# Kernel optimization log

Measured on AMD Instinct MI355X. Metric: run time of the kernel, lower is better.

The kernel has to match this reference:

```python
import jax, jax.numpy as jnp
import numpy as np

B, T, N, NF, H, C, E = 4, 16, 4096, 8, 64, 13, 131072
NUM_HEADS = 4


def setup_inputs() -> dict:
    key = jax.random.key(0)
    ks = jax.random.split(key, 32)
    s = 0.05

    def w(k, shape):
        return (jax.random.normal(k, shape, jnp.float32) * s)

    p = {}
    p["node_features"] = jax.random.normal(ks[0], (B, T, N, NF), jnp.float32)
    p["edge_index_seq"] = jax.random.randint(ks[1], (T, 2, E), 0, N)
    # spatial_conv: Linear(NF,H) -> ReLU -> Linear(H,H)
    p["sc_w1"] = w(ks[2], (H, NF)); p["sc_b1"] = w(ks[3], (H,))
    p["sc_w2"] = w(ks[4], (H, H)); p["sc_b2"] = w(ks[5], (H,))
    # 2-layer LSTM (eval mode, dropout inactive); gate order i,f,g,o
    p["w_ih0"] = w(ks[6], (4 * H, H)); p["w_hh0"] = w(ks[7], (4 * H, H))
    p["b_ih0"] = w(ks[8], (4 * H,)); p["b_hh0"] = w(ks[9], (4 * H,))
    p["w_ih1"] = w(ks[10], (4 * H, H)); p["w_hh1"] = w(ks[11], (4 * H, H))
    p["b_ih1"] = w(ks[12], (4 * H,)); p["b_hh1"] = w(ks[13], (4 * H,))
    # MultiheadAttention (packed in-proj like torch)
    p["attn_in_w"] = w(ks[14], (3 * H, H)); p["attn_in_b"] = w(ks[15], (3 * H,))
    p["attn_out_w"] = w(ks[16], (H, H)); p["attn_out_b"] = w(ks[17], (H,))
    # predictor MLP (dropout inactive in eval)
    p["pw1"] = w(ks[18], (2 * H, H)); p["pb1"] = w(ks[19], (2 * H,))
    p["pw2"] = w(ks[20], (H, 2 * H)); p["pb2"] = w(ks[21], (H,))
    p["pw3"] = w(ks[22], (C, H)); p["pb3"] = w(ks[23], (C,))
    return p


def _message_pass(h_t, edges, n_nodes):
    # h_t: [B, N, H]; edges: [2, E]
    src, dst = edges[0], edges[1]
    msgs = h_t[:, src, :]  # gather pre-update embeddings, [B, E, H]
    sums = jax.vmap(lambda m: jax.ops.segment_sum(m, dst, num_segments=n_nodes))(msgs)
    cnt = jax.ops.segment_sum(jnp.ones(dst.shape, h_t.dtype), dst, num_segments=n_nodes)
    mean = sums / jnp.maximum(cnt, 1.0)[None, :, None]
    has_msg = (cnt > 0)[None, :, None]
    return jnp.where(has_msg, (h_t + mean) * 0.5, h_t)


def _lstm_layer(x, wi, wh, bi, bh):
    # x: [M, T, H] -> [M, T, H]
    M = x.shape[0]
    Hh = wh.shape[1]
    xg = x @ wi.T + bi  # precompute input contribution, [M, T, 4H]
    def step(carry, xg_t):
        hp, cp = carry
        g = xg_t + hp @ wh.T + bh
        i, f, gg, o = jnp.split(g, 4, axis=-1)
        i = jax.nn.sigmoid(i); f = jax.nn.sigmoid(f)
        gg = jnp.tanh(gg); o = jax.nn.sigmoid(o)
        c = f * cp + i * gg
        hn = o * jnp.tanh(c)
        return (hn, c), hn
    init = (jnp.zeros((M, Hh), x.dtype), jnp.zeros((M, Hh), x.dtype))
    _, hs = jax.lax.scan(step, init, xg.transpose(1, 0, 2))
    return hs.transpose(1, 0, 2)


def reference(node_features, edge_index_seq, sc_w1, sc_b1, sc_w2, sc_b2,
              w_ih0, w_hh0, b_ih0, b_hh0, w_ih1, w_hh1, b_ih1, b_hh1,
              attn_in_w, attn_in_b, attn_out_w, attn_out_b,
              pw1, pb1, pw2, pb2, pw3, pb3):
    Bs, Ts, Ns, _ = node_features.shape
    Hh = sc_w1.shape[0]

    # spatial conv over all timesteps at once: [B, T, N, H]
    h = jax.nn.relu(node_features @ sc_w1.T + sc_b1) @ sc_w2.T + sc_b2

    # per-timestep gather + segment-mean message passing (memory-bound core)
    def step(_, inp):
        h_t, e_t = inp
        return None, _message_pass(h_t, e_t, Ns)
    _, h_mp = jax.lax.scan(step, None, (h.transpose(1, 0, 2, 3), edge_index_seq))
    spatial_stack = h_mp.transpose(1, 0, 2, 3)  # [B, T, N, H]

    # LSTM over time per (batch, node)
    x = spatial_stack.transpose(0, 2, 1, 3).reshape(Bs * Ns, Ts, Hh)
    x = _lstm_layer(x, w_ih0, w_hh0, b_ih0, b_hh0)
    x = _lstm_layer(x, w_ih1, w_hh1, b_ih1, b_hh1)

    # self-attention (torch MHA, batch_first)
    qkv = x @ attn_in_w.T + attn_in_b
    q, k, v = jnp.split(qkv, 3, axis=-1)
    hd = Hh // NUM_HEADS
    def heads(z):
        return z.reshape(Bs * Ns, Ts, NUM_HEADS, hd).transpose(0, 2, 1, 3)
    q, k, v = heads(q), heads(k), heads(v)
    scores = jnp.einsum('mhqd,mhkd->mhqk', q, k) / np.float32(np.sqrt(hd))
    attn = jax.nn.softmax(scores, axis=-1)
    o = jnp.einsum('mhqk,mhkd->mhqd', attn, v)
    o = o.transpose(0, 2, 1, 3).reshape(Bs * Ns, Ts, Hh)
    o = o @ attn_out_w.T + attn_out_b

    final_hidden = o[:, -1, :]
    z = jax.nn.relu(final_hidden @ pw1.T + pb1)
    z = jax.nn.relu(z @ pw2.T + pb2)
    logits = z @ pw3.T + pb3
    return logits.reshape(Bs, Ns, -1)
```

## Files before the change

kernel.cpp:

```cpp
#include <hip/hip_runtime.h>

#define Bq 4
#define Tq 16
#define Nq 4096
#define NFq 8
#define Hq 64
#define Eq 131072
#define Cq 13
#define Mq (Bq*Nq)

typedef __attribute__((ext_vector_type(8))) short bf16x8;
typedef __attribute__((ext_vector_type(4))) float f32x4;

__device__ __forceinline__ float bf2f(unsigned short u) {
  return __uint_as_float(((unsigned int)u) << 16);
}
__device__ __forceinline__ unsigned short f2bf(float f) {
  unsigned int x = __float_as_uint(f);
  unsigned int r = x + 0x7fff + ((x >> 16) & 1);
  return (unsigned short)(r >> 16);
}
__device__ __forceinline__ float rcpf(float x) {
  float r;
  asm("v_rcp_f32 %0, %1" : "=v"(r) : "v"(x));
  return r;
}
__device__ __forceinline__ float sigf(float x) {
  return rcpf(1.f + __expf(-x));
}
__device__ __forceinline__ float tanh_c(float x) {
  float e = __expf(-2.f * x);
  return 2.f * rcpf(1.f + e) - 1.f;
}
__device__ __forceinline__ unsigned int pk_bf16(float lo, float hi) {
  unsigned int r;
  asm("v_cvt_pk_bf16_f32 %0, %1, %2" : "=v"(r) : "v"(lo), "v"(hi));
  return r;
}
__device__ __forceinline__ float dot2bf(unsigned int a, unsigned int b, float c) {
  float r;
  asm("v_dot2_f32_bf16 %0, %1, %2, %3" : "=v"(r) : "v"(a), "v"(b), "v"(c));
  return r;
}

#define O_BC0  65536
#define O_BC1  65792
#define O_QB   70144
#define O_VB   74304
#define O_B1P  95872

#define WB_AQT  0
#define WB_AWK  4096
#define WB_WVT  8192
#define WB_P1OW 12288
#define WB_P2T  20480
#define WB_P3T  28672
#define WB_TOT  29696

#define AQT_P   0
#define WVT_P   2048
#define P1OW_P  4096
#define P2T_P   8192
#define WAVE_SCR 3648
#define SMEM_ATTN (49152 + 8 * WAVE_SCR)

__global__ __launch_bounds__(256) void k_prep(
    const float* __restrict__ bih0, const float* __restrict__ bhh0,
    const float* __restrict__ bih1, const float* __restrict__ bhh1,
    float* __restrict__ wT) {
  int i = threadIdx.x;
  wT[O_BC0 + i] = bih0[i] + bhh0[i];
  wT[O_BC1 + i] = bih1[i] + bhh1[i];
}

__global__ __launch_bounds__(256) void k_prep_wa(
    const float* __restrict__ wih0, const float* __restrict__ whh0,
    const float* __restrict__ wih1, const float* __restrict__ whh1,
    unsigned short* __restrict__ WA) {
  int i = blockIdx.x * 256 + threadIdx.x;
  int j = i & 7, lane = (i >> 3) & 63, ks = (i >> 9) & 3;
  int mt = (i >> 11) & 15, L = (i >> 15) & 1;
  int rp = 16 * mt + (lane & 15);
  int orig = (rp & 3) * 64 + (rp >> 2);
  int k = 32 * ks + 8 * (lane >> 4) + j;
  const float* w = L ? (k < 64 ? wih1 : whh1) : (k < 64 ? wih0 : whh0);
  WA[i] = f2bf(w[orig * 64 + (k & 63)]);
}

__global__ __launch_bounds__(256) void k_prep2(
    const float* __restrict__ aw, const float* __restrict__ ab,
    const float* __restrict__ pw2, const float* __restrict__ pw3,
    unsigned short* __restrict__ WBu, float* __restrict__ wT) {
  int i = blockIdx.x * 256 + threadIdx.x;
  if (i < 4096) {
    int k = i >> 6, ch = i & 63;
    int pidx = (k >> 1) * 128 + ch * 2 + (k & 1);
    WBu[WB_AQT + pidx] = f2bf(0.25f * aw[ch * 64 + k]);
    WBu[WB_AWK + i]    = f2bf(aw[(64 + k) * 64 + ch]);
    WBu[WB_WVT + pidx] = f2bf(aw[(128 + ch) * 64 + k]);
  }
  {
    int k = i >> 6, j = i & 63;
    int pidx = (k >> 1) * 128 + j * 2 + (k & 1);
    WBu[WB_P2T + pidx] = f2bf(pw2[j * 128 + k]);
  }
  if (i < 1024) {
    int k = i >> 4, c = i & 15;
    int pidx = (k >> 1) * 32 + c * 2 + (k & 1);
    WBu[WB_P3T + pidx] = (c < 13) ? f2bf(pw3[c * 64 + k]) : (unsigned short)0;
  }
  if (i < 64) {
    wT[O_QB + i] = 0.25f * ab[i];
    wT[O_VB + i] = ab[128 + i];
  }
}

__global__ __launch_bounds__(256) void k_prep3(
    const float* __restrict__ pw1, const float* __restrict__ ow,
    const float* __restrict__ ob, const float* __restrict__ pb1,
    unsigned short* __restrict__ WBu, float* __restrict__ wT) {
  int i = blockIdx.x * 256 + threadIdx.x;
  int j = i >> 6, k = i & 63;
  float s0 = 0.f, s1 = 0.f, s2 = 0.f, s3 = 0.f;
  for (int m2 = 0; m2 < 64; m2 += 4) {
    s0 += pw1[j * 64 + m2]     * ow[m2 * 64 + k];
    s1 += pw1[j * 64 + m2 + 1] * ow[(m2 + 1) * 64 + k];
    s2 += pw1[j * 64 + m2 + 2] * ow[(m2 + 2) * 64 + k];
    s3 += pw1[j * 64 + m2 + 3] * ow[(m2 + 3) * 64 + k];
  }
  WBu[WB_P1OW + (k >> 1) * 256 + j * 2 + (k & 1)] = f2bf((s0 + s1) + (s2 + s3));
  if (k == 0) {
    float b = pb1[j];
    for (int m2 = 0; m2 < 64; ++m2) b += pw1[j * 64 + m2] * ob[m2];
    wT[O_B1P + j] = b;
  }
}

__global__ __launch_bounds__(256) void k_enc(
    const float* __restrict__ nf, const float* __restrict__ w1,
    const float* __restrict__ b1, const float* __restrict__ w2,
    const float* __restrict__ b2, unsigned short* __restrict__ henc) {
  __shared__ float xr[64][9];
  __shared__ float w1l[64][8];
  __shared__ float b1l[64];
  __shared__ float w2l[4096];
  __shared__ float b2l[64];
  __shared__ float h1l[64 * 65];
  __shared__ unsigned short OUT[64 * 68];
  int tid = threadIdx.x;
  size_t row0 = (size_t)blockIdx.x * 64;
  if (tid < 128) {
    float4 v = ((const float4*)w1)[tid];
    int j = tid >> 1, q = tid & 1;
    w1l[j][q * 4] = v.x; w1l[j][q * 4 + 1] = v.y;
    w1l[j][q * 4 + 2] = v.z; w1l[j][q * 4 + 3] = v.w;
  }
  if (tid < 64) { b1l[tid] = b1[tid]; b2l[tid] = b2[tid]; }
  {
    const float4* s = (const float4*)w2;
    #pragma unroll
    for (int u = 0; u < 4; ++u) {
      float4 v = s[tid + u * 256];
      int base = (tid + u * 256) * 4;
      w2l[base] = v.x; w2l[base + 1] = v.y; w2l[base + 2] = v.z; w2l[base + 3] = v.w;
    }
  }
  if (tid < 128) {
    float4 v = ((const float4*)(nf + row0 * 8))[tid];
    int r = tid >> 1, q = tid & 1;
    xr[r][q * 4] = v.x; xr[r][q * 4 + 1] = v.y;
    xr[r][q * 4 + 2] = v.z; xr[r][q * 4 + 3] = v.w;
  }
  __syncthreads();
  int r = tid & 63, co = tid >> 6;
  #pragma unroll
  for (int jj = 0; jj < 16; ++jj) {
    int j = co * 16 + jj;
    float acc = b1l[j];
    #pragma unroll
    for (int k = 0; k < 8; ++k) acc += w1l[j][k] * xr[r][k];
    h1l[r * 65 + j] = fmaxf(acc, 0.f);
  }
  __syncthreads();
  float acc[16];
  #pragma unroll
  for (int jj = 0; jj < 16; ++jj) acc[jj] = b2l[co * 16 + jj];
  for (int k = 0; k < 64; ++k) {
    float xv = h1l[r * 65 + k];
    #pragma unroll
    for (int jj = 0; jj < 16; ++jj)
      acc[jj] += w2l[(co * 16 + jj) * 64 + k] * xv;
  }
  #pragma unroll
  for (int jj = 0; jj < 16; jj += 2) {
    unsigned int pk = (unsigned int)f2bf(acc[jj]) | ((unsigned int)f2bf(acc[jj + 1]) << 16);
    *(unsigned int*)(&OUT[r * 68 + co * 16 + jj]) = pk;
  }
  __syncthreads();
  {
    int rr = tid >> 2, part = tid & 3;
    uint2 a = *(uint2*)(&OUT[rr * 68 + part * 16]);
    uint2 b = *(uint2*)(&OUT[rr * 68 + part * 16 + 4]);
    uint4 v; v.x = a.x; v.y = a.y; v.z = b.x; v.w = b.y;
    *(uint4*)(henc + (row0 + rr) * 64 + part * 16) = v;
  }
}

__global__ __launch_bounds__(1024) void k_count(const int* __restrict__ ei,
                                                int* __restrict__ bhist) {
  __shared__ int hist[4096];
  int b = blockIdx.x;
  int t = b & 15, seg = b >> 4;
  int tid = threadIdx.x;
  #pragma unroll
  for (int i = tid; i < 4096; i += 1024) hist[i] = 0;
  __syncthreads();
  const int* dstp = ei + ((t << 1) + 1) * Eq + (seg << 13);
  #pragma unroll
  for (int u = 0; u < 8; ++u) {
    int dst = dstp[(u << 10) + tid];
    atomicAdd(&hist[dst], 1);
  }
  __syncthreads();
  int* op = bhist + (b << 12);
  #pragma unroll
  for (int i = tid; i < 4096; i += 1024) op[i] = hist[i];
}

__global__ __launch_bounds__(256) void k_scan(const int* __restrict__ bhist,
                                              int* __restrict__ rp,
                                              int* __restrict__ segoff) {
  int t = blockIdx.x, tid = threadIdx.x;
  __shared__ int part[256];
  int loc[16];
  int s = 0;
  #pragma unroll
  for (int j = 0; j < 16; ++j) {
    int node = tid * 16 + j;
    int v = 0;
    #pragma unroll
    for (int seg = 0; seg < 16; ++seg)
      v += bhist[((t + (seg << 4)) << 12) + node];
    loc[j] = v;
    s += v;
  }
  part[tid] = s;
  __syncthreads();
  if (tid == 0) {
    int run = 0;
    for (int i2 = 0; i2 < 256; ++i2) { int v = part[i2]; part[i2] = run; run += v; }
  }
  __syncthreads();
  int off = part[tid];
  #pragma unroll
  for (int j = 0; j < 16; ++j) {
    int node = tid * 16 + j;
    rp[t * (Nq + 1) + node] = off;
    int running = off;
    #pragma unroll
    for (int seg = 0; seg < 16; ++seg) {
      segoff[(((t << 4) + seg) << 12) + node] = running;
      running += bhist[((t + (seg << 4)) << 12) + node];
    }
    off += loc[j];
  }
  if (tid == 255) rp[t * (Nq + 1) + Nq] = off;
}

__global__ __launch_bounds__(1024) void k_scatter(const int* __restrict__ ei,
    const int* __restrict__ segoff, int* __restrict__ col) {
  __shared__ int loff[4096];
  int b = blockIdx.x;
  int t = b & 15, seg = b >> 4;
  int tid = threadIdx.x;
  for (int i = tid; i < 4096; i += 1024)
    loff[i] = segoff[(((t << 4) + seg) << 12) + i];
  __syncthreads();
  const int* srcp = ei + (t << 1) * Eq + (seg << 13);
  const int* dstp = ei + ((t << 1) + 1) * Eq + (seg << 13);
  #pragma unroll
  for (int u = 0; u < 8; ++u) {
    int e = (u << 10) + tid;
    int src = srcp[e];
    int dst = dstp[e];
    int pos = atomicAdd(&loff[dst], 1);
    col[(t << 17) + pos] = src;
  }
}

__global__ __launch_bounds__(256) void k_mp(const unsigned short* __restrict__ henc,
    const int* __restrict__ rp, const int* __restrict__ col,
    unsigned short* __restrict__ hmp) {
  int lane = threadIdx.x & 63;
  int bkk = blockIdx.x;
  int t = bkk & 15;
  int n = (bkk >> 4) * 4 + __builtin_amdgcn_readfirstlane(threadIdx.x >> 6);
  const int* rpt = rp + t * (Nq + 1);
  const int* colt = col + (t << 17);
  int e0 = rpt[n], e1 = rpt[n + 1];
  int half = lane >> 5;
  int b2 = (lane >> 3) & 3;
  int c8 = (lane & 7) << 3;
  const unsigned short* hb2 = henc + (size_t)b2 * 4194304 + t * 262144 + c8;
  float acc[8] = {0.f, 0.f, 0.f, 0.f, 0.f, 0.f, 0.f, 0.f};
  int e = e0;
  for (; e + 8 <= e1; e += 8) {
    int i0 = colt[e + half];
    int i1 = colt[e + 2 + half];
    int i2 = colt[e + 4 + half];
    int i3 = colt[e + 6 + half];
    uint4 p0 = *(const uint4*)(hb2 + i0 * 64);
    uint4 p1 = *(const uint4*)(hb2 + i1 * 64);
    uint4 p2 = *(const uint4*)(hb2 + i2 * 64);
    uint4 p3 = *(const uint4*)(hb2 + i3 * 64);
    acc[0] += bf2f((unsigned short)(p0.x & 0xffff)) + bf2f((unsigned short)(p1.x & 0xffff))
            + bf2f((unsigned short)(p2.x & 0xffff)) + bf2f((unsigned short)(p3.x & 0xffff));
    acc[1] += bf2f((unsigned short)(p0.x >> 16)) + bf2f((unsigned short)(p1.x >> 16))
            + bf2f((unsigned short)(p2.x >> 16)) + bf2f((unsigned short)(p3.x >> 16));
    acc[2] += bf2f((unsigned short)(p0.y & 0xffff)) + bf2f((unsigned short)(p1.y & 0xffff))
            + bf2f((unsigned short)(p2.y & 0xffff)) + bf2f((unsigned short)(p3.y & 0xffff));
    acc[3] += bf2f((unsigned short)(p0.y >> 16)) + bf2f((unsigned short)(p1.y >> 16))
            + bf2f((unsigned short)(p2.y >> 16)) + bf2f((unsigned short)(p3.y >> 16));
    acc[4] += bf2f((unsigned short)(p0.z & 0xffff)) + bf2f((unsigned short)(p1.z & 0xffff))
            + bf2f((unsigned short)(p2.z & 0xffff)) + bf2f((unsigned short)(p3.z & 0xffff));
    acc[5] += bf2f((unsigned short)(p0.z >> 16)) + bf2f((unsigned short)(p1.z >> 16))
            + bf2f((unsigned short)(p2.z >> 16)) + bf2f((unsigned short)(p3.z >> 16));
    acc[6] += bf2f((unsigned short)(p0.w & 0xffff)) + bf2f((unsigned short)(p1.w & 0xffff))
            + bf2f((unsigned short)(p2.w & 0xffff)) + bf2f((unsigned short)(p3.w & 0xffff));
    acc[7] += bf2f((unsigned short)(p0.w >> 16)) + bf2f((unsigned short)(p1.w >> 16))
            + bf2f((unsigned short)(p2.w >> 16)) + bf2f((unsigned short)(p3.w >> 16));
  }
  if (half == 0) {
    for (; e < e1; ++e) {
      int i0 = colt[e];
      uint4 p0 = *(const uint4*)(hb2 + i0 * 64);
      acc[0] += bf2f((unsigned short)(p0.x & 0xffff));
      acc[1] += bf2f((unsigned short)(p0.x >> 16));
      acc[2] += bf2f((unsigned short)(p0.y & 0xffff));
      acc[3] += bf2f((unsigned short)(p0.y >> 16));
      acc[4] += bf2f((unsigned short)(p0.z & 0xffff));
      acc[5] += bf2f((unsigned short)(p0.z >> 16));
      acc[6] += bf2f((unsigned short)(p0.w & 0xffff));
      acc[7] += bf2f((unsigned short)(p0.w >> 16));
    }
  }
  #pragma unroll
  for (int i = 0; i < 8; ++i) acc[i] += __shfl_xor(acc[i], 32);
  uint4 ps = *(const uint4*)(hb2 + n * 64);
  int deg = e1 - e0;
  if (half == 0) {
    uint4 out;
    if (deg > 0) {
      float sc = 0.5f * rcpf((float)deg);
      float s0 = bf2f((unsigned short)(ps.x & 0xffff)) * 0.5f + acc[0] * sc;
      float s1 = bf2f((unsigned short)(ps.x >> 16))    * 0.5f + acc[1] * sc;
      float s2 = bf2f((unsigned short)(ps.y & 0xffff)) * 0.5f + acc[2] * sc;
      float s3 = bf2f((unsigned short)(ps.y >> 16))    * 0.5f + acc[3] * sc;
      float s4 = bf2f((unsigned short)(ps.z & 0xffff)) * 0.5f + acc[4] * sc;
      float s5 = bf2f((unsigned short)(ps.z >> 16))    * 0.5f + acc[5] * sc;
      float s6 = bf2f((unsigned short)(ps.w & 0xffff)) * 0.5f + acc[6] * sc;
      float s7 = bf2f((unsigned short)(ps.w >> 16))    * 0.5f + acc[7] * sc;
      out.x = pk_bf16(s0, s1);
      out.y = pk_bf16(s2, s3);
      out.z = pk_bf16(s4, s5);
      out.w = pk_bf16(s6, s7);
    } else {
      out = ps;
    }
    *(uint4*)(hmp + (size_t)b2 * 4194304 + t * 262144 + n * 64 + c8) = out;
  }
}

__global__ __launch_bounds__(1024) void k_lstm(
    const unsigned short* __restrict__ hmp,
    const unsigned short* __restrict__ WA,
    const float* __restrict__ wT,
    unsigned short* __restrict__ x2) {
  __shared__ unsigned short XF[2][4096];
  __shared__ unsigned short H0F[2][4096];
  __shared__ unsigned short H1F[2][4096];
  __shared__ unsigned short OUTB[64 * 68];
  int tid = threadIdx.x;
  int l = tid & 63;
  int w = tid >> 6;
  int mtp = w >> 1, ntp = w & 1;
  int m0 = blockIdx.x << 6;

  bf16x8 afr[2][2][4];
  const bf16x8* wa8 = (const bf16x8*)WA;
  #pragma unroll
  for (int L = 0; L < 2; ++L)
    #pragma unroll
    for (int mt2 = 0; mt2 < 2; ++mt2)
      #pragma unroll
      for (int ks = 0; ks < 4; ++ks)
        afr[L][mt2][ks] = wa8[((L * 16 + (2 * mtp + mt2)) * 4 + ks) * 64 + l];

  float4 bias0[2], bias1[2];
  int hbase[2], obase[2];
  #pragma unroll
  for (int mt2 = 0; mt2 < 2; ++mt2) {
    int ch = 4 * (2 * mtp + mt2) + (l >> 4);
    bias0[mt2].x = wT[O_BC0 + ch];       bias0[mt2].y = wT[O_BC0 + 64 + ch];
    bias0[mt2].z = wT[O_BC0 + 128 + ch]; bias0[mt2].w = wT[O_BC0 + 192 + ch];
    bias1[mt2].x = wT[O_BC1 + ch];       bias1[mt2].y = wT[O_BC1 + 64 + ch];
    bias1[mt2].z = wT[O_BC1 + 128 + ch]; bias1[mt2].w = wT[O_BC1 + 192 + ch];
    int l2 = (l & 15) | (((ch >> 3) & 3) << 4);
    hbase[mt2] = (ch >> 5) * 2048 + l2 * 8 + (ch & 7);
    obase[mt2] = (l & 15) * 68 + ch;
  }
  float c0a[2][2] = {{0.f, 0.f}, {0.f, 0.f}};
  float c1a[2][2] = {{0.f, 0.f}, {0.f, 0.f}};

  int sA = tid >> 4, c4 = (tid & 15) << 2;
  int xfidx = (((c4 >> 5) * 4 + (sA >> 4)) * 64 + ((sA & 15) | (((c4 >> 3) & 3) << 4))) * 8 + (c4 & 7);
  int mm = m0 + sA;
  int bb = mm >> 12, nn = mm & 4095;
  const unsigned short* srcb = hmp + ((size_t)(bb * 16) * 4096 + (size_t)nn) * 64 + c4;
  unsigned short* x2g = x2 + (size_t)mm * (Tq * Hq) + c4;
  int outsrc = sA * 68 + c4;

  int* hz0 = (int*)&H0F[1][0];
  int* hz1 = (int*)&H1F[1][0];
  for (int i = tid; i < 2048; i += 1024) { hz0[i] = 0; hz1[i] = 0; }

  uint2 xv = *(const uint2*)srcb;
  *(uint2*)(&XF[0][0] + xfidx) = xv;
  __syncthreads();

  for (int t = 0; t < Tq; ++t) {
    int cur = t & 1, prv = cur ^ 1;

    if (t > 0) {
      uint2 ov = *(const uint2*)(OUTB + outsrc);
      *(uint2*)(x2g + (t - 1) * 64) = ov;
    }
    if (t < Tq - 1) xv = *(const uint2*)(srcb + (t + 1) * 262144);
    {
      f32x4 acc[2][2];
      #pragma unroll
      for (int mt2 = 0; mt2 < 2; ++mt2)
        #pragma unroll
        for (int nt2 = 0; nt2 < 2; ++nt2) {
          float4 bv = bias0[mt2];
          acc[mt2][nt2] = (f32x4){bv.x, bv.y, bv.z, bv.w};
        }
      #pragma unroll
      for (int nt2 = 0; nt2 < 2; ++nt2) {
        int nt = 2 * ntp + nt2;
        #pragma unroll
        for (int ks = 0; ks < 4; ++ks) {
          const unsigned short* bs = (ks < 2) ? &XF[cur][0] : &H0F[prv][0];
          bf16x8 bf = *(const bf16x8*)(bs + (((ks & 1) * 4 + nt) * 64 + l) * 8);
          acc[0][nt2] = __builtin_amdgcn_mfma_f32_16x16x32_bf16(afr[0][0][ks], bf, acc[0][nt2], 0, 0, 0);
          acc[1][nt2] = __builtin_amdgcn_mfma_f32_16x16x32_bf16(afr[0][1][ks], bf, acc[1][nt2], 0, 0, 0);
        }
      }
      #pragma unroll
      for (int mt2 = 0; mt2 < 2; ++mt2) {
        float hh[2];
        #pragma unroll
        for (int nt2 = 0; nt2 < 2; ++nt2) {
          f32x4 g = acc[mt2][nt2];
          float ig = sigf(g[0]);
          float fg = sigf(g[1]);
          float gg = tanh_c(g[2]);
          float og = sigf(g[3]);
          float c = fg * c0a[mt2][nt2] + ig * gg;
          c0a[mt2][nt2] = c;
          hh[nt2] = og * tanh_c(c);
        }
        unsigned int pk = pk_bf16(hh[0], hh[1]);
        int base = hbase[mt2] + 2 * ntp * 512;
        H0F[cur][base]       = (unsigned short)pk;
        H0F[cur][base + 512] = (unsigned short)(pk >> 16);
      }
    }
    __syncthreads();

    {
      f32x4 acc[2][2];
      #pragma unroll
      for (int mt2 = 0; mt2 < 2; ++mt2)
        #pragma unroll
        for (int nt2 = 0; nt2 < 2; ++nt2) {
          float4 bv = bias1[mt2];
          acc[mt2][nt2] = (f32x4){bv.x, bv.y, bv.z, bv.w};
        }
      #pragma unroll
      for (int nt2 = 0; nt2 < 2; ++nt2) {
        int nt = 2 * ntp + nt2;
        #pragma unroll
        for (int ks = 0; ks < 4; ++ks) {
          const unsigned short* bs = (ks < 2) ? &H0F[cur][0] : &H1F[prv][0];
          bf16x8 bf = *(const bf16x8*)(bs + (((ks & 1) * 4 + nt) * 64 + l) * 8);
          acc[0][nt2] = __builtin_amdgcn_mfma_f32_16x16x32_bf16(afr[1][0][ks], bf, acc[0][nt2], 0, 0, 0);
          acc[1][nt2] = __builtin_amdgcn_mfma_f32_16x16x32_bf16(afr[1][1][ks], bf, acc[1][nt2], 0, 0, 0);
        }
      }
      #pragma unroll
      for (int mt2 = 0; mt2 < 2; ++mt2) {
        float hh[2];
        #pragma unroll
        for (int nt2 = 0; nt2 < 2; ++nt2) {
          f32x4 g = acc[mt2][nt2];
          float ig = sigf(g[0]);
          float fg = sigf(g[1]);
          float gg = tanh_c(g[2]);
          float og = sigf(g[3]);
          float c = fg * c1a[mt2][nt2] + ig * gg;
          c1a[mt2][nt2] = c;
          hh[nt2] = og * tanh_c(c);
        }
        unsigned int pk = pk_bf16(hh[0], hh[1]);
        int base = hbase[mt2] + 2 * ntp * 512;
        H1F[cur][base]       = (unsigned short)pk;
        H1F[cur][base + 512] = (unsigned short)(pk >> 16);
        int ob = obase[mt2] + 2 * ntp * 1088;
        OUTB[ob]        = (unsigned short)pk;
        OUTB[ob + 1088] = (unsigned short)(pk >> 16);
      }
    }
    if (t < Tq - 1) *(uint2*)(&XF[prv][0] + xfidx) = xv;
    __syncthreads();
  }
  {
    uint2 ov = *(const uint2*)(OUTB + outsrc);
    *(uint2*)(x2g + (Tq - 1) * 64) = ov;
  }
}

__global__ __launch_bounds__(512, 4) void k_attn(const unsigned short* __restrict__ x2,
    const unsigned short* __restrict__ WB, const float* __restrict__ wp,
    const float* __restrict__ pb2, const float* __restrict__ pb3,
    float* __restrict__ outp) {
  extern __shared__ char smem[];
  unsigned int* WLu = (unsigned int*)smem;
  int tid = threadIdx.x;
  int lane = tid & 63;
  int wid = tid >> 6;
  {
    const uint4* src = (const uint4*)WB;
    uint4* dstw = (uint4*)smem;
    for (int i = tid; i < 3072; i += 512)
      dstw[i] = src[(i < 512) ? i : i + 512];
  }
  char* wbase = smem + 49152 + wid * WAVE_SCR;
  unsigned short* xw = (unsigned short*)wbase;
  float* q = (float*)(wbase + 2304);
  unsigned int* op = (unsigned int*)(wbase + 2304);
  unsigned int* qkp = (unsigned int*)(wbase + 2560);
  unsigned int* hbp = qkp;
  float* pz = (float*)(wbase + 3104);
  unsigned int* z2p = (unsigned int*)(wbase + 3104);
  unsigned int* z1p = (unsigned int*)(wbase + 3360);
  int m = (blockIdx.x << 3) + wid;
  {
    const uint4* xp = (const uint4*)(x2 + (size_t)m * 1024);
    #pragma unroll
    for (int u = 0; u < 2; ++u) {
      uint4 pv = xp[lane * 2 + u];
      int f0 = (lane * 2 + u) * 8;
      int t = f0 >> 6, ch0 = f0 & 63;
      *(uint4*)(xw + t * 72 + ch0) = pv;
    }
  }
  __syncthreads();
  {
    const unsigned short* xr = xw + 15 * 72;
    float a0 = wp[O_QB + lane], a1 = 0.f, a2 = 0.f, a3 = 0.f;
    #pragma unroll
    for (int k2 = 0; k2 < 32; k2 += 4) {
      a0 = dot2bf(WLu[AQT_P + (k2 + 0) * 64 + lane], *(const unsigned int*)(xr + 2 * (k2 + 0)), a0);
      a1 = dot2bf(WLu[AQT_P + (k2 + 1) * 64 + lane], *(const unsigned int*)(xr + 2 * (k2 + 1)), a1);
      a2 = dot2bf(WLu[AQT_P + (k2 + 2) * 64 + lane], *(const unsigned int*)(xr + 2 * (k2 + 2)), a2);
      a3 = dot2bf(WLu[AQT_P + (k2 + 3) * 64 + lane], *(const unsigned int*)(xr + 2 * (k2 + 3)), a3);
    }
    q[lane] = (a0 + a1) + (a2 + a3);
  }
  #pragma unroll
  for (int h = 0; h < 4; ++h) {
    float a0 = 0.f, a1 = 0.f, a2 = 0.f, a3 = 0.f;
    #pragma unroll
    for (int d = 0; d < 16; d += 4) {
      a0 += bf2f(WB[WB_AWK + (h * 16 + d + 0) * 64 + lane]) * q[h * 16 + d + 0];
      a1 += bf2f(WB[WB_AWK + (h * 16 + d + 1) * 64 + lane]) * q[h * 16 + d + 1];
      a2 += bf2f(WB[WB_AWK + (h * 16 + d + 2) * 64 + lane]) * q[h * 16 + d + 2];
      a3 += bf2f(WB[WB_AWK + (h * 16 + d + 3) * 64 + lane]) * q[h * 16 + d + 3];
    }
    float a = (a0 + a1) + (a2 + a3);
    float an = __shfl_xor(a, 1);
    if (!(lane & 1)) qkp[h * 33 + (lane >> 1)] = pk_bf16(a, an);
  }
  {
    int hh = lane >> 4, tt = lane & 15;
    const unsigned short* xr = xw + tt * 72;
    float a0 = 0.f, a1 = 0.f, a2 = 0.f, a3 = 0.f;
    #pragma unroll
    for (int c2 = 0; c2 < 32; c2 += 4) {
      a0 = dot2bf(qkp[hh * 33 + c2 + 0], *(const unsigned int*)(xr + 2 * (c2 + 0)), a0);
      a1 = dot2bf(qkp[hh * 33 + c2 + 1], *(const unsigned int*)(xr + 2 * (c2 + 1)), a1);
      a2 = dot2bf(qkp[hh * 33 + c2 + 2], *(const unsigned int*)(xr + 2 * (c2 + 2)), a2);
      a3 = dot2bf(qkp[hh * 33 + c2 + 3], *(const unsigned int*)(xr + 2 * (c2 + 3)), a3);
    }
    float sc = (a0 + a1) + (a2 + a3);
    float mx = sc;
    mx = fmaxf(mx, __shfl_xor(mx, 1));
    mx = fmaxf(mx, __shfl_xor(mx, 2));
    mx = fmaxf(mx, __shfl_xor(mx, 4));
    mx = fmaxf(mx, __shfl_xor(mx, 8));
    float e = __expf(sc - mx);
    float sum = e;
    sum += __shfl_xor(sum, 1);
    sum += __shfl_xor(sum, 2);
    sum += __shfl_xor(sum, 4);
    sum += __shfl_xor(sum, 8);
    pz[lane] = e * rcpf(sum);
  }
  {
    float hb0 = 0.f, hb1 = 0.f, hb2 = 0.f, hb3 = 0.f;
    #pragma unroll
    for (int t = 0; t < 16; ++t) {
      float xv = bf2f(xw[t * 72 + lane]);
      hb0 += pz[t] * xv;
      hb1 += pz[16 + t] * xv;
      hb2 += pz[32 + t] * xv;
      hb3 += pz[48 + t] * xv;
    }
    float n0 = __shfl_xor(hb0, 1);
    float n1 = __shfl_xor(hb1, 1);
    float n2 = __shfl_xor(hb2, 1);
    float n3 = __shfl_xor(hb3, 1);
    if (!(lane & 1)) {
      int p = lane >> 1;
      hbp[p]          = pk_bf16(hb0, n0);
      hbp[33 + p]     = pk_bf16(hb1, n1);
      hbp[66 + p]     = pk_bf16(hb2, n2);
      hbp[99 + p]     = pk_bf16(hb3, n3);
    }
  }
  {
    int hsel = lane >> 4;
    float a0 = wp[O_VB + lane], a1 = 0.f, a2 = 0.f, a3 = 0.f;
    #pragma unroll
    for (int k2 = 0; k2 < 32; k2 += 4) {
      a0 = dot2bf(WLu[WVT_P + (k2 + 0) * 64 + lane], hbp[hsel * 33 + k2 + 0], a0);
      a1 = dot2bf(WLu[WVT_P + (k2 + 1) * 64 + lane], hbp[hsel * 33 + k2 + 1], a1);
      a2 = dot2bf(WLu[WVT_P + (k2 + 2) * 64 + lane], hbp[hsel * 33 + k2 + 2], a2);
      a3 = dot2bf(WLu[WVT_P + (k2 + 3) * 64 + lane], hbp[hsel * 33 + k2 + 3], a3);
    }
    float o = (a0 + a1) + (a2 + a3);
    float on = __shfl_xor(o, 1);
    if (!(lane & 1)) op[lane >> 1] = pk_bf16(o, on);
  }
  {
    float a0 = wp[O_B1P + lane], a1 = 0.f;
    float b0 = wp[O_B1P + 64 + lane], b1 = 0.f;
    #pragma unroll
    for (int k2 = 0; k2 < 32; k2 += 2) {
      unsigned int ov0 = op[k2], ov1 = op[k2 + 1];
      a0 = dot2bf(WLu[P1OW_P + (k2 + 0) * 128 + lane], ov0, a0);
      a1 = dot2bf(WLu[P1OW_P + (k2 + 1) * 128 + lane], ov1, a1);
      b0 = dot2bf(WLu[P1OW_P + (k2 + 0) * 128 + 64 + lane], ov0, b0);
      b1 = dot2bf(WLu[P1OW_P + (k2 + 1) * 128 + 64 + lane], ov1, b1);
    }
    float ra = fmaxf(a0 + a1, 0.f);
    float rb = fmaxf(b0 + b1, 0.f);
    float ran = __shfl_xor(ra, 1);
    float rbn = __shfl_xor(rb, 1);
    if (!(lane & 1)) {
      z1p[lane >> 1]      = pk_bf16(ra, ran);
      z1p[32 + (lane >> 1)] = pk_bf16(rb, rbn);
    }
  }
  {
    float a0 = pb2[lane], a1 = 0.f, a2 = 0.f, a3 = 0.f;
    #pragma unroll
    for (int k2 = 0; k2 < 64; k2 += 4) {
      a0 = dot2bf(WLu[P2T_P + (k2 + 0) * 64 + lane], z1p[k2 + 0], a0);
      a1 = dot2bf(WLu[P2T_P + (k2 + 1) * 64 + lane], z1p[k2 + 1], a1);
      a2 = dot2bf(WLu[P2T_P + (k2 + 2) * 64 + lane], z1p[k2 + 2], a2);
      a3 = dot2bf(WLu[P2T_P + (k2 + 3) * 64 + lane], z1p[k2 + 3], a3);
    }
    float z2 = fmaxf((a0 + a1) + (a2 + a3), 0.f);
    float zn = __shfl_xor(z2, 1);
    if (!(lane & 1)) z2p[lane >> 1] = pk_bf16(z2, zn);
  }
  {
    const unsigned int* p3 = (const unsigned int*)(WB + WB_P3T);
    int c = lane & 15;
    float a0 = (c < 13) ? pb3[c] : 0.f, a1 = 0.f, a2 = 0.f, a3 = 0.f;
    #pragma unroll
    for (int k2 = 0; k2 < 32; k2 += 4) {
      a0 = dot2bf(p3[(k2 + 0) * 16 + c], z2p[k2 + 0], a0);
      a1 = dot2bf(p3[(k2 + 1) * 16 + c], z2p[k2 + 1], a1);
      a2 = dot2bf(p3[(k2 + 2) * 16 + c], z2p[k2 + 2], a2);
      a3 = dot2bf(p3[(k2 + 3) * 16 + c], z2p[k2 + 3], a3);
    }
    if (lane < 13) outp[(size_t)m * 13 + lane] = (a0 + a1) + (a2 + a3);
  }
}

extern "C" void kernel_launch(void* const* d_in, const int* in_sizes, int n_in,
                              void* d_out, int out_size, void* d_ws, size_t ws_size,
                              hipStream_t stream) {
  (void)in_sizes; (void)n_in; (void)out_size; (void)ws_size;
  const float* nf   = (const float*)d_in[0];
  const int*   ei   = (const int*)d_in[1];
  const float* sw1  = (const float*)d_in[2];
  const float* sb1  = (const float*)d_in[3];
  const float* sw2  = (const float*)d_in[4];
  const float* sb2  = (const float*)d_in[5];
  const float* wih0 = (const float*)d_in[6];
  const float* whh0 = (const float*)d_in[7];
  const float* bih0 = (const float*)d_in[8];
  const float* bhh0 = (const float*)d_in[9];
  const float* wih1 = (const float*)d_in[10];
  const float* whh1 = (const float*)d_in[11];
  const float* bih1 = (const float*)d_in[12];
  const float* bhh1 = (const float*)d_in[13];
  const float* aw   = (const float*)d_in[14];
  const float* ab   = (const float*)d_in[15];
  const float* ow   = (const float*)d_in[16];
  const float* ob   = (const float*)d_in[17];
  const float* pw1  = (const float*)d_in[18];
  const float* pb1  = (const float*)d_in[19];
  const float* pw2  = (const float*)d_in[20];
  const float* pb2  = (const float*)d_in[21];
  const float* pw3  = (const float*)d_in[22];
  const float* pb3  = (const float*)d_in[23];

  char* ws = (char*)d_ws;
  float* wT = (float*)ws;
  unsigned short* WA = (unsigned short*)(ws + 393216);
  unsigned short* WB = (unsigned short*)(ws + 458752);
  int* rp   = (int*)(ws + 1048576);
  int* col  = (int*)(ws + 1572864);
  unsigned short* henc = (unsigned short*)(ws + 10485760);
  unsigned short* hmp  = (unsigned short*)(ws + 44040192);
  int* bhist  = (int*)(ws + 44040192);
  int* segoff = (int*)(ws + 48234496);
  unsigned short* x2   = henc;
  float* outp = (float*)d_out;

  hipFuncSetAttribute((const void*)k_attn,
                      hipFuncAttributeMaxDynamicSharedMemorySize, SMEM_ATTN);
  k_prep<<<1, 256, 0, stream>>>(bih0, bhh0, bih1, bhh1, wT);
  k_prep_wa<<<256, 256, 0, stream>>>(wih0, whh0, wih1, whh1, WA);
  k_prep2<<<32, 256, 0, stream>>>(aw, ab, pw2, pw3, WB, wT);
  k_prep3<<<32, 256, 0, stream>>>(pw1, ow, ob, pb1, WB, wT);
  k_enc<<<4096, 256, 0, stream>>>(nf, sw1, sb1, sw2, sb2, henc);
  k_count<<<256, 1024, 0, stream>>>(ei, bhist);
  k_scan<<<16, 256, 0, stream>>>(bhist, rp, segoff);
  k_scatter<<<256, 1024, 0, stream>>>(ei, segoff, col);
  k_mp<<<16384, 256, 0, stream>>>(henc, rp, col, hmp);
  k_lstm<<<256, 1024, 0, stream>>>(hmp, WA, wT, x2);
  k_attn<<<2048, 512, SMEM_ATTN, stream>>>(x2, WB, wT, pb2, pb3, outp);
}
```

Baseline: 282.7 us.

## Run spatial encoder second linear layer on bf16 MFMA with prepacked weights

```diff
diff --git a/kernel.cpp b/kernel.cpp
--- a/kernel.cpp
+++ b/kernel.cpp
@@ -90,7 +90,9 @@
 __global__ __launch_bounds__(256) void k_prep2(
     const float* __restrict__ aw, const float* __restrict__ ab,
     const float* __restrict__ pw2, const float* __restrict__ pw3,
-    unsigned short* __restrict__ WBu, float* __restrict__ wT) {
+    const float* __restrict__ sw2,
+    unsigned short* __restrict__ WBu, unsigned short* __restrict__ WE,
+    float* __restrict__ wT) {
   int i = blockIdx.x * 256 + threadIdx.x;
   if (i < 4096) {
     int k = i >> 6, ch = i & 63;
@@ -98,6 +100,8 @@
     WBu[WB_AQT + pidx] = f2bf(0.25f * aw[ch * 64 + k]);
     WBu[WB_AWK + i]    = f2bf(aw[(64 + k) * 64 + ch]);
     WBu[WB_WVT + pidx] = f2bf(aw[(128 + ch) * 64 + k]);
+    int e = i & 7, l = (i >> 3) & 63, eks = (i >> 9) & 1, mt = i >> 10;
+    WE[i] = f2bf(sw2[(mt * 16 + (l & 15)) * 64 + 32 * eks + 8 * (l >> 4) + e]);
   }
   {
     int k = i >> 6, j = i & 63;
@@ -138,71 +142,80 @@
 
 __global__ __launch_bounds__(256) void k_enc(
     const float* __restrict__ nf, const float* __restrict__ w1,
-    const float* __restrict__ b1, const float* __restrict__ w2,
+    const float* __restrict__ b1, const unsigned short* __restrict__ WE,
     const float* __restrict__ b2, unsigned short* __restrict__ henc) {
   __shared__ float xr[64][9];
-  __shared__ float w1l[64][8];
-  __shared__ float b1l[64];
-  __shared__ float w2l[4096];
-  __shared__ float b2l[64];
-  __shared__ float h1l[64 * 65];
-  __shared__ unsigned short OUT[64 * 68];
+  __shared__ unsigned short H1F[4096];
+  __shared__ unsigned short OUT[64 * 72];
   int tid = threadIdx.x;
+  int lane = tid & 63;
+  int wv = tid >> 6;
   size_t row0 = (size_t)blockIdx.x * 64;
-  if (tid < 128) {
-    float4 v = ((const float4*)w1)[tid];
-    int j = tid >> 1, q = tid & 1;
-    w1l[j][q * 4] = v.x; w1l[j][q * 4 + 1] = v.y;
-    w1l[j][q * 4 + 2] = v.z; w1l[j][q * 4 + 3] = v.w;
-  }
-  if (tid < 64) { b1l[tid] = b1[tid]; b2l[tid] = b2[tid]; }
-  {
-    const float4* s = (const float4*)w2;
-    #pragma unroll
-    for (int u = 0; u < 4; ++u) {
-      float4 v = s[tid + u * 256];
-      int base = (tid + u * 256) * 4;
-      w2l[base] = v.x; w2l[base + 1] = v.y; w2l[base + 2] = v.z; w2l[base + 3] = v.w;
-    }
-  }
-  if (tid < 128) {
-    float4 v = ((const float4*)(nf + row0 * 8))[tid];
-    int r = tid >> 1, q = tid & 1;
-    xr[r][q * 4] = v.x; xr[r][q * 4 + 1] = v.y;
-    xr[r][q * 4 + 2] = v.z; xr[r][q * 4 + 3] = v.w;
-  }
-  __syncthreads();
-  int r = tid & 63, co = tid >> 6;
-  #pragma unroll
-  for (int jj = 0; jj < 16; ++jj) {
-    int j = co * 16 + jj;
-    float acc = b1l[j];
-    #pragma unroll
-    for (int k = 0; k < 8; ++k) acc += w1l[j][k] * xr[r][k];
-    h1l[r * 65 + j] = fmaxf(acc, 0.f);
-  }
-  __syncthreads();
-  float acc[16];
-  #pragma unroll
-  for (int jj = 0; jj < 16; ++jj) acc[jj] = b2l[co * 16 + jj];
-  for (int k = 0; k < 64; ++k) {
-    float xv = h1l[r * 65 + k];
-    #pragma unroll
-    for (int jj = 0; jj < 16; ++jj)
-      acc[jj] += w2l[(co * 16 + jj) * 64 + k] * xv;
-  }
-  #pragma unroll
-  for (int jj = 0; jj < 16; jj += 2) {
-    unsigned int pk = (unsigned int)f2bf(acc[jj]) | ((unsigned int)f2bf(acc[jj + 1]) << 16);
-    *(unsigned int*)(&OUT[r * 68 + co * 16 + jj]) = pk;
+  {
+    float2 v = ((const float2*)(nf + row0 * 8))[tid];
+    int r = tid >> 2, q = tid & 3;
+    xr[r][q * 2] = v.x;
+    xr[r][q * 2 + 1] = v.y;
+  }
+  bf16x8 afr0, afr1;
+  {
+    const bf16x8* we8 = (const bf16x8*)WE;
+    afr0 = we8[(wv * 2 + 0) * 64 + lane];
+    afr1 = we8[(wv * 2 + 1) * 64 + lane];
+  }
+  int chb = wv * 16 + (lane >> 4) * 4;
+  float4 b2v;
+  b2v.x = b2[chb]; b2v.y = b2[chb + 1]; b2v.z = b2[chb + 2]; b2v.w = b2[chb + 3];
+  __syncthreads();
+  {
+    int r = lane;
+    float x0 = xr[r][0], x1 = xr[r][1], x2v = xr[r][2], x3 = xr[r][3];
+    float x4 = xr[r][4], x5 = xr[r][5], x6 = xr[r][6], x7 = xr[r][7];
+    #pragma unroll
+    for (int run = 0; run < 2; ++run) {
+      unsigned int pk4[4];
+      #pragma unroll
+      for (int p = 0; p < 4; ++p) {
+        int j0 = wv * 16 + run * 8 + p * 2;
+        const float* wr0 = w1 + j0 * 8;
+        const float* wr1 = wr0 + 8;
+        float a0 = b1[j0]     + wr0[0]*x0 + wr0[1]*x1 + wr0[2]*x2v + wr0[3]*x3
+                              + wr0[4]*x4 + wr0[5]*x5 + wr0[6]*x6 + wr0[7]*x7;
+        float a1 = b1[j0 + 1] + wr1[0]*x0 + wr1[1]*x1 + wr1[2]*x2v + wr1[3]*x3
+                              + wr1[4]*x4 + wr1[5]*x5 + wr1[6]*x6 + wr1[7]*x7;
+        pk4[p] = pk_bf16(fmaxf(a0, 0.f), fmaxf(a1, 0.f));
+      }
+      int jb = wv * 16 + run * 8;
+      int ks = jb >> 5;
+      int l2 = (r & 15) | (((jb >> 3) & 3) << 4);
+      int nt = r >> 4;
+      uint4 v; v.x = pk4[0]; v.y = pk4[1]; v.z = pk4[2]; v.w = pk4[3];
+      *(uint4*)(&H1F[((ks * 4 + nt) * 64 + l2) * 8]) = v;
+    }
+  }
+  __syncthreads();
+  {
+    #pragma unroll
+    for (int nt = 0; nt < 4; ++nt) {
+      f32x4 acc = (f32x4){b2v.x, b2v.y, b2v.z, b2v.w};
+      bf16x8 bf0 = *(const bf16x8*)(&H1F[((0 * 4 + nt) * 64 + lane) * 8]);
+      bf16x8 bf1 = *(const bf16x8*)(&H1F[((1 * 4 + nt) * 64 + lane) * 8]);
+      acc = __builtin_amdgcn_mfma_f32_16x16x32_bf16(afr0, bf0, acc, 0, 0, 0);
+      acc = __builtin_amdgcn_mfma_f32_16x16x32_bf16(afr1, bf1, acc, 0, 0, 0);
+      int orow = nt * 16 + (lane & 15);
+      uint2 pv;
+      pv.x = pk_bf16(acc[0], acc[1]);
+      pv.y = pk_bf16(acc[2], acc[3]);
+      *(uint2*)(&OUT[orow * 72 + chb]) = pv;
+    }
   }
   __syncthreads();
   {
     int rr = tid >> 2, part = tid & 3;
-    uint2 a = *(uint2*)(&OUT[rr * 68 + part * 16]);
-    uint2 b = *(uint2*)(&OUT[rr * 68 + part * 16 + 4]);
-    uint4 v; v.x = a.x; v.y = a.y; v.z = b.x; v.w = b.y;
-    *(uint4*)(henc + (row0 + rr) * 64 + part * 16) = v;
+    uint4 v0 = *(uint4*)(&OUT[rr * 72 + part * 16]);
+    uint4 v1 = *(uint4*)(&OUT[rr * 72 + part * 16 + 8]);
+    *(uint4*)(henc + (row0 + rr) * 64 + part * 16) = v0;
+    *(uint4*)(henc + (row0 + rr) * 64 + part * 16 + 8) = v1;
   }
 }
 
@@ -734,6 +747,7 @@
   float* wT = (float*)ws;
   unsigned short* WA = (unsigned short*)(ws + 393216);
   unsigned short* WB = (unsigned short*)(ws + 458752);
+  unsigned short* WE = (unsigned short*)(ws + 520192);
   int* rp   = (int*)(ws + 1048576);
   int* col  = (int*)(ws + 1572864);
   unsigned short* henc = (unsigned short*)(ws + 10485760);
@@ -747,9 +761,9 @@
                       hipFuncAttributeMaxDynamicSharedMemorySize, SMEM_ATTN);
   k_prep<<<1, 256, 0, stream>>>(bih0, bhh0, bih1, bhh1, wT);
   k_prep_wa<<<256, 256, 0, stream>>>(wih0, whh0, wih1, whh1, WA);
-  k_prep2<<<32, 256, 0, stream>>>(aw, ab, pw2, pw3, WB, wT);
+  k_prep2<<<32, 256, 0, stream>>>(aw, ab, pw2, pw3, sw2, WB, WE, wT);
   k_prep3<<<32, 256, 0, stream>>>(pw1, ow, ob, pb1, WB, wT);
-  k_enc<<<4096, 256, 0, stream>>>(nf, sw1, sb1, sw2, sb2, henc);
+  k_enc<<<4096, 256, 0, stream>>>(nf, sw1, sb1, WE, sb2, henc);
   k_count<<<256, 1024, 0, stream>>>(ei, bhist);
   k_scan<<<16, 256, 0, stream>>>(bhist, rp, segoff);
   k_scatter<<<256, 1024, 0, stream>>>(ei, segoff, col);
```

After: 252.4 us. -10.7%, faster.
